# Kernel tuning notes

Measured on AMD Instinct MI355X. Metric: run time of the kernel, lower is better.

## Reference

```python
import jax, jax.numpy as jnp
import numpy as np

MAX_TOKENS = 8192
MAX_NUM_NODES = 8192
FEATURES = 256


def setup_inputs() -> dict:
    key = jax.random.key(0)
    k_emb, k_start, k_end = jax.random.split(key, 3)
    embedding = jax.random.normal(k_emb, (MAX_NUM_NODES, FEATURES), dtype=jnp.float32)
    node_span_starts = jax.random.randint(k_start, (MAX_NUM_NODES,), 0, 4096, dtype=jnp.int32)
    node_span_ends = jax.random.randint(k_end, (MAX_NUM_NODES,), 0, MAX_TOKENS, dtype=jnp.int32)
    return {
        "embedding": embedding,
        "node_span_starts": node_span_starts,
        "node_span_ends": node_span_ends,
        "num_nodes": 6000,
    }


def reference(embedding, node_span_starts, node_span_ends, num_nodes):
    # For each token t: out[t] = sum over valid nodes n with start_n <= t <= end_n of embedding[n].
    # Identical math to the original vmap+where+sum, expressed as a masked matmul
    # to avoid the O(N*T*F) dense intermediate.
    t = jnp.arange(MAX_TOKENS)[:, None]                      # [T, 1]
    node_valid = jnp.arange(MAX_NUM_NODES) < num_nodes       # [N]
    in_span = (node_span_starts[None, :] <= t) & (t <= node_span_ends[None, :])  # [T, N]
    mask = (in_span & node_valid[None, :]).astype(embedding.dtype)               # [T, N]
    return mask @ embedding                                  # [T, F]
```

## Files before the change

### kernel.cpp

```cpp
#include <hip/hip_runtime.h>

#define T_TOKENS 8192
#define MAX_NODES 8192
#define FEAT 256
#define NCHUNKS 1024
#define CHUNK 8
#define NSUPER 32
#define SUPER 32
#define LIST_CAP 4096
#define EV_STRIDE LIST_CAP

__global__ __launch_bounds__(FEAT) void classify_colsum_kernel(
    const float* __restrict__ emb,
    const int* __restrict__ starts,
    const int* __restrict__ ends,
    const int* __restrict__ num_nodes_p,
    float* __restrict__ colsum,
    float* __restrict__ supersum,
    int* __restrict__ evcnt,
    int* __restrict__ evbuf) {
    __shared__ int s_list[LIST_CAP];
    __shared__ int s_cnt;
    const int c = blockIdx.x;
    const int tid = threadIdx.x;
    const int f = tid;
    const int num_nodes = *num_nodes_p;
    const int row_lo = c * CHUNK;
    const int row_hi = row_lo + CHUNK;
    const int4* starts4 = (const int4*)starts;
    const int4* ends4 = (const int4*)ends;

    if (tid == 0) s_cnt = 0;
    __syncthreads();
#pragma unroll
    for (int r = 0; r < MAX_NODES / (4 * FEAT); ++r) {
        const int vec = r * FEAT + tid;
        const int4 s4 = starts4[vec];
        const int4 e4 = ends4[vec];
        const int sv[4] = {s4.x, s4.y, s4.z, s4.w};
        const int ev[4] = {e4.x, e4.y, e4.z, e4.w};
        const int nb = vec * 4;
#pragma unroll
        for (int k = 0; k < 4; ++k) {
            const int node = nb + k;
            const int s = sv[k];
            const int e = ev[k];
            if (node < num_nodes && s <= e && s < T_TOKENS && e >= 0) {
                const int sc = s < 0 ? 0 : s;
                if (sc >= row_lo && sc < row_hi) {
                    int p = atomicAdd(&s_cnt, 1);
                    if (p < LIST_CAP) s_list[p] = (node << 4) | ((sc - row_lo) << 1);
                }
                const int e1 = e + 1;
                if (e1 < T_TOKENS && e1 >= row_lo && e1 < row_hi) {
                    int p = atomicAdd(&s_cnt, 1);
                    if (p < LIST_CAP) s_list[p] = (node << 4) | ((e1 - row_lo) << 1) | 1;
                }
            }
        }
    }
    __syncthreads();
    const int cnt = min(s_cnt, LIST_CAP);

    int* evb = evbuf + (size_t)c * EV_STRIDE;
    for (int j = tid; j < cnt; j += FEAT) evb[j] = s_list[j];
    if (tid == 0) evcnt[c] = cnt;

    float acc = 0.f;
    int j = 0;
    for (; j + 8 <= cnt; j += 8) {
        const int e0 = s_list[j + 0], e1 = s_list[j + 1];
        const int e2 = s_list[j + 2], e3 = s_list[j + 3];
        const int e4_ = s_list[j + 4], e5 = s_list[j + 5];
        const int e6 = s_list[j + 6], e7 = s_list[j + 7];
        const float v0 = emb[(size_t)(e0 >> 4) * FEAT + f];
        const float v1 = emb[(size_t)(e1 >> 4) * FEAT + f];
        const float v2 = emb[(size_t)(e2 >> 4) * FEAT + f];
        const float v3 = emb[(size_t)(e3 >> 4) * FEAT + f];
        const float v4 = emb[(size_t)(e4_ >> 4) * FEAT + f];
        const float v5 = emb[(size_t)(e5 >> 4) * FEAT + f];
        const float v6 = emb[(size_t)(e6 >> 4) * FEAT + f];
        const float v7 = emb[(size_t)(e7 >> 4) * FEAT + f];
        acc += (e0 & 1) ? -v0 : v0;
        acc += (e1 & 1) ? -v1 : v1;
        acc += (e2 & 1) ? -v2 : v2;
        acc += (e3 & 1) ? -v3 : v3;
        acc += (e4_ & 1) ? -v4 : v4;
        acc += (e5 & 1) ? -v5 : v5;
        acc += (e6 & 1) ? -v6 : v6;
        acc += (e7 & 1) ? -v7 : v7;
    }
    for (; j < cnt; ++j) {
        const int e0 = s_list[j];
        const float v0 = emb[(size_t)(e0 >> 4) * FEAT + f];
        acc += (e0 & 1) ? -v0 : v0;
    }
    colsum[(size_t)c * FEAT + f] = acc;
    atomicAdd(&supersum[(size_t)(c >> 5) * FEAT + f], acc);
}

#define APPLY_EVENT(eV, vV)                          \
    {                                                \
        const float sv_ = ((eV) & 1) ? -(vV) : (vV); \
        const int lr_ = ((eV) >> 1) & 7;             \
        d0 += (lr_ == 0) ? sv_ : 0.f;                \
        d1 += (lr_ == 1) ? sv_ : 0.f;                \
        d2 += (lr_ == 2) ? sv_ : 0.f;                \
        d3 += (lr_ == 3) ? sv_ : 0.f;                \
        d4 += (lr_ == 4) ? sv_ : 0.f;                \
        d5 += (lr_ == 5) ? sv_ : 0.f;                \
        d6 += (lr_ == 6) ? sv_ : 0.f;                \
        d7 += (lr_ == 7) ? sv_ : 0.f;                \
    }

__global__ __launch_bounds__(FEAT) void scan_kernel(
    const float* __restrict__ emb,
    const float* __restrict__ colsum,
    const float* __restrict__ supersum,
    const int* __restrict__ evcnt,
    const int* __restrict__ evbuf,
    float* __restrict__ out) {
    const int c = blockIdx.x;
    const int f = threadIdx.x;
    const int sg = c >> 5;

    const int cnt = evcnt[c];
    const int* evb = evbuf + (size_t)c * EV_STRIDE;

    float r0 = 0.f, r1 = 0.f, r2 = 0.f, r3 = 0.f;
    float r4 = 0.f, r5 = 0.f, r6 = 0.f, r7 = 0.f;
    int i = 0;
    for (; i + 8 <= sg; i += 8) {
        r0 += supersum[(size_t)(i + 0) * FEAT + f];
        r1 += supersum[(size_t)(i + 1) * FEAT + f];
        r2 += supersum[(size_t)(i + 2) * FEAT + f];
        r3 += supersum[(size_t)(i + 3) * FEAT + f];
        r4 += supersum[(size_t)(i + 4) * FEAT + f];
        r5 += supersum[(size_t)(i + 5) * FEAT + f];
        r6 += supersum[(size_t)(i + 6) * FEAT + f];
        r7 += supersum[(size_t)(i + 7) * FEAT + f];
    }
    for (; i < sg; ++i) r0 += supersum[(size_t)i * FEAT + f];
    i = sg * SUPER;
    for (; i + 8 <= c; i += 8) {
        r0 += colsum[(size_t)(i + 0) * FEAT + f];
        r1 += colsum[(size_t)(i + 1) * FEAT + f];
        r2 += colsum[(size_t)(i + 2) * FEAT + f];
        r3 += colsum[(size_t)(i + 3) * FEAT + f];
        r4 += colsum[(size_t)(i + 4) * FEAT + f];
        r5 += colsum[(size_t)(i + 5) * FEAT + f];
        r6 += colsum[(size_t)(i + 6) * FEAT + f];
        r7 += colsum[(size_t)(i + 7) * FEAT + f];
    }
    for (; i < c; ++i) r0 += colsum[(size_t)i * FEAT + f];
    float run = ((r0 + r1) + (r2 + r3)) + ((r4 + r5) + (r6 + r7));

    float d0 = 0.f, d1 = 0.f, d2 = 0.f, d3 = 0.f;
    float d4 = 0.f, d5 = 0.f, d6 = 0.f, d7 = 0.f;
    int j = 0;
    for (; j + 4 <= cnt; j += 4) {
        const int e0 = evb[j + 0], e1 = evb[j + 1];
        const int e2 = evb[j + 2], e3 = evb[j + 3];
        const float v0 = emb[(size_t)(e0 >> 4) * FEAT + f];
        const float v1 = emb[(size_t)(e1 >> 4) * FEAT + f];
        const float v2 = emb[(size_t)(e2 >> 4) * FEAT + f];
        const float v3 = emb[(size_t)(e3 >> 4) * FEAT + f];
        APPLY_EVENT(e0, v0);
        APPLY_EVENT(e1, v1);
        APPLY_EVENT(e2, v2);
        APPLY_EVENT(e3, v3);
    }
    for (; j < cnt; ++j) {
        const int e0 = evb[j];
        const float v0 = emb[(size_t)(e0 >> 4) * FEAT + f];
        APPLY_EVENT(e0, v0);
    }

    float* o = out + (size_t)c * CHUNK * FEAT + f;
    run += d0; o[0 * FEAT] = run;
    run += d1; o[1 * FEAT] = run;
    run += d2; o[2 * FEAT] = run;
    run += d3; o[3 * FEAT] = run;
    run += d4; o[4 * FEAT] = run;
    run += d5; o[5 * FEAT] = run;
    run += d6; o[6 * FEAT] = run;
    run += d7; o[7 * FEAT] = run;
}

extern "C" void kernel_launch(void* const* d_in, const int* in_sizes, int n_in,
                              void* d_out, int out_size, void* d_ws, size_t ws_size,
                              hipStream_t stream) {
    const float* emb     = (const float*)d_in[0];
    const int* starts    = (const int*)d_in[1];
    const int* ends      = (const int*)d_in[2];
    const int* num_nodes = (const int*)d_in[3];
    float* out           = (float*)d_out;

    float* colsum   = (float*)d_ws;
    float* supersum = colsum + (size_t)NCHUNKS * FEAT;
    int* evcnt      = (int*)(supersum + (size_t)NSUPER * FEAT);
    int* evbuf      = evcnt + NCHUNKS;

    hipMemsetAsync(supersum, 0, (size_t)NSUPER * FEAT * sizeof(float), stream);

    classify_colsum_kernel<<<NCHUNKS, FEAT, 0, stream>>>(
        emb, starts, ends, num_nodes, colsum, supersum, evcnt, evbuf);
    scan_kernel<<<NCHUNKS, FEAT, 0, stream>>>(
        emb, colsum, supersum, evcnt, evbuf, out);
}
```

Before: 84.19 us.

## Fuse classify and scan into one cooperative kernel with grid syncs

Replaces the memset plus two-kernel pipeline with a single cooperative kernel. Each block keeps its event list in shared memory and its per-row deltas in registers, so it no longer writes events to global memory, re-reads them, or gathers embedding rows a second time. Supersums are computed after a grid sync instead of with atomics. The trade-off is two grid-wide barriers and a requirement that all 1024 blocks be co-resident; if the occupancy check or the cooperative launch fails, it falls back to the old path.

```diff
diff --git a/kernel.cpp b/kernel.cpp
--- a/kernel.cpp
+++ b/kernel.cpp
@@ -1,4 +1,7 @@
 #include <hip/hip_runtime.h>
+#include <hip/hip_cooperative_groups.h>
+
+namespace cg = cooperative_groups;
 
 #define T_TOKENS 8192
 #define MAX_NODES 8192
@@ -9,6 +12,167 @@
 #define SUPER 32
 #define LIST_CAP 4096
 #define EV_STRIDE LIST_CAP
+
+#define APPLY_EVENT(eV, vV)                          \
+    {                                                \
+        const float sv_ = ((eV) & 1) ? -(vV) : (vV); \
+        const int lr_ = ((eV) >> 1) & 7;             \
+        d0 += (lr_ == 0) ? sv_ : 0.f;                \
+        d1 += (lr_ == 1) ? sv_ : 0.f;                \
+        d2 += (lr_ == 2) ? sv_ : 0.f;                \
+        d3 += (lr_ == 3) ? sv_ : 0.f;                \
+        d4 += (lr_ == 4) ? sv_ : 0.f;                \
+        d5 += (lr_ == 5) ? sv_ : 0.f;                \
+        d6 += (lr_ == 6) ? sv_ : 0.f;                \
+        d7 += (lr_ == 7) ? sv_ : 0.f;                \
+    }
+
+__global__ __launch_bounds__(FEAT, 4) void fused_kernel(
+    const float* __restrict__ emb,
+    const int* __restrict__ starts,
+    const int* __restrict__ ends,
+    const int* __restrict__ num_nodes_p,
+    float* __restrict__ colsum,
+    float* __restrict__ supersum,
+    float* __restrict__ out) {
+    __shared__ int s_list[LIST_CAP];
+    __shared__ int s_cnt;
+    const int c = blockIdx.x;
+    const int tid = threadIdx.x;
+    const int f = tid;
+    const int num_nodes = *num_nodes_p;
+    const int row_lo = c * CHUNK;
+    const int row_hi = row_lo + CHUNK;
+    const int4* starts4 = (const int4*)starts;
+    const int4* ends4 = (const int4*)ends;
+
+    if (tid == 0) s_cnt = 0;
+    __syncthreads();
+#pragma unroll
+    for (int r = 0; r < MAX_NODES / (4 * FEAT); ++r) {
+        const int vec = r * FEAT + tid;
+        const int4 s4 = starts4[vec];
+        const int4 e4 = ends4[vec];
+        const int sv[4] = {s4.x, s4.y, s4.z, s4.w};
+        const int ev[4] = {e4.x, e4.y, e4.z, e4.w};
+        const int nb = vec * 4;
+#pragma unroll
+        for (int k = 0; k < 4; ++k) {
+            const int node = nb + k;
+            const int s = sv[k];
+            const int e = ev[k];
+            if (node < num_nodes && s <= e && s < T_TOKENS && e >= 0) {
+                const int sc = s < 0 ? 0 : s;
+                if (sc >= row_lo && sc < row_hi) {
+                    int p = atomicAdd(&s_cnt, 1);
+                    if (p < LIST_CAP) s_list[p] = (node << 4) | ((sc - row_lo) << 1);
+                }
+                const int e1 = e + 1;
+                if (e1 < T_TOKENS && e1 >= row_lo && e1 < row_hi) {
+                    int p = atomicAdd(&s_cnt, 1);
+                    if (p < LIST_CAP) s_list[p] = (node << 4) | ((e1 - row_lo) << 1) | 1;
+                }
+            }
+        }
+    }
+    __syncthreads();
+    const int cnt = min(s_cnt, LIST_CAP);
+
+    float d0 = 0.f, d1 = 0.f, d2 = 0.f, d3 = 0.f;
+    float d4 = 0.f, d5 = 0.f, d6 = 0.f, d7 = 0.f;
+    {
+        int j = 0;
+        for (; j + 8 <= cnt; j += 8) {
+            const int e0 = s_list[j + 0], e1 = s_list[j + 1];
+            const int e2 = s_list[j + 2], e3 = s_list[j + 3];
+            const int e4_ = s_list[j + 4], e5 = s_list[j + 5];
+            const int e6 = s_list[j + 6], e7 = s_list[j + 7];
+            const float v0 = emb[(size_t)(e0 >> 4) * FEAT + f];
+            const float v1 = emb[(size_t)(e1 >> 4) * FEAT + f];
+            const float v2 = emb[(size_t)(e2 >> 4) * FEAT + f];
+            const float v3 = emb[(size_t)(e3 >> 4) * FEAT + f];
+            const float v4 = emb[(size_t)(e4_ >> 4) * FEAT + f];
+            const float v5 = emb[(size_t)(e5 >> 4) * FEAT + f];
+            const float v6 = emb[(size_t)(e6 >> 4) * FEAT + f];
+            const float v7 = emb[(size_t)(e7 >> 4) * FEAT + f];
+            APPLY_EVENT(e0, v0);
+            APPLY_EVENT(e1, v1);
+            APPLY_EVENT(e2, v2);
+            APPLY_EVENT(e3, v3);
+            APPLY_EVENT(e4_, v4);
+            APPLY_EVENT(e5, v5);
+            APPLY_EVENT(e6, v6);
+            APPLY_EVENT(e7, v7);
+        }
+        for (; j < cnt; ++j) {
+            const int e0 = s_list[j];
+            const float v0 = emb[(size_t)(e0 >> 4) * FEAT + f];
+            APPLY_EVENT(e0, v0);
+        }
+    }
+    colsum[(size_t)c * FEAT + f] = ((d0 + d1) + (d2 + d3)) + ((d4 + d5) + (d6 + d7));
+
+    cg::this_grid().sync();
+
+    if (c < NSUPER) {
+        const float* cs = colsum + (size_t)c * SUPER * FEAT + f;
+        float t0 = 0.f, t1 = 0.f, t2 = 0.f, t3 = 0.f;
+        float t4 = 0.f, t5 = 0.f, t6 = 0.f, t7 = 0.f;
+#pragma unroll
+        for (int j = 0; j < SUPER; j += 8) {
+            t0 += cs[(size_t)(j + 0) * FEAT];
+            t1 += cs[(size_t)(j + 1) * FEAT];
+            t2 += cs[(size_t)(j + 2) * FEAT];
+            t3 += cs[(size_t)(j + 3) * FEAT];
+            t4 += cs[(size_t)(j + 4) * FEAT];
+            t5 += cs[(size_t)(j + 5) * FEAT];
+            t6 += cs[(size_t)(j + 6) * FEAT];
+            t7 += cs[(size_t)(j + 7) * FEAT];
+        }
+        supersum[(size_t)c * FEAT + f] = ((t0 + t1) + (t2 + t3)) + ((t4 + t5) + (t6 + t7));
+    }
+
+    cg::this_grid().sync();
+
+    const int sg = c >> 5;
+    float r0 = 0.f, r1 = 0.f, r2 = 0.f, r3 = 0.f;
+    float r4 = 0.f, r5 = 0.f, r6 = 0.f, r7 = 0.f;
+    int i = 0;
+    for (; i + 8 <= sg; i += 8) {
+        r0 += supersum[(size_t)(i + 0) * FEAT + f];
+        r1 += supersum[(size_t)(i + 1) * FEAT + f];
+        r2 += supersum[(size_t)(i + 2) * FEAT + f];
+        r3 += supersum[(size_t)(i + 3) * FEAT + f];
+        r4 += supersum[(size_t)(i + 4) * FEAT + f];
+        r5 += supersum[(size_t)(i + 5) * FEAT + f];
+        r6 += supersum[(size_t)(i + 6) * FEAT + f];
+        r7 += supersum[(size_t)(i + 7) * FEAT + f];
+    }
+    for (; i < sg; ++i) r0 += supersum[(size_t)i * FEAT + f];
+    i = sg * SUPER;
+    for (; i + 8 <= c; i += 8) {
+        r0 += colsum[(size_t)(i + 0) * FEAT + f];
+        r1 += colsum[(size_t)(i + 1) * FEAT + f];
+        r2 += colsum[(size_t)(i + 2) * FEAT + f];
+        r3 += colsum[(size_t)(i + 3) * FEAT + f];
+        r4 += colsum[(size_t)(i + 4) * FEAT + f];
+        r5 += colsum[(size_t)(i + 5) * FEAT + f];
+        r6 += colsum[(size_t)(i + 6) * FEAT + f];
+        r7 += colsum[(size_t)(i + 7) * FEAT + f];
+    }
+    for (; i < c; ++i) r0 += colsum[(size_t)i * FEAT + f];
+    float run = ((r0 + r1) + (r2 + r3)) + ((r4 + r5) + (r6 + r7));
+
+    float* o = out + (size_t)c * CHUNK * FEAT + f;
+    run += d0; o[0 * FEAT] = run;
+    run += d1; o[1 * FEAT] = run;
+    run += d2; o[2 * FEAT] = run;
+    run += d3; o[3 * FEAT] = run;
+    run += d4; o[4 * FEAT] = run;
+    run += d5; o[5 * FEAT] = run;
+    run += d6; o[6 * FEAT] = run;
+    run += d7; o[7 * FEAT] = run;
+}
 
 __global__ __launch_bounds__(FEAT) void classify_colsum_kernel(
     const float* __restrict__ emb,
@@ -99,20 +263,6 @@
     atomicAdd(&supersum[(size_t)(c >> 5) * FEAT + f], acc);
 }
 
-#define APPLY_EVENT(eV, vV)                          \
-    {                                                \
-        const float sv_ = ((eV) & 1) ? -(vV) : (vV); \
-        const int lr_ = ((eV) >> 1) & 7;             \
-        d0 += (lr_ == 0) ? sv_ : 0.f;                \
-        d1 += (lr_ == 1) ? sv_ : 0.f;                \
-        d2 += (lr_ == 2) ? sv_ : 0.f;                \
-        d3 += (lr_ == 3) ? sv_ : 0.f;                \
-        d4 += (lr_ == 4) ? sv_ : 0.f;                \
-        d5 += (lr_ == 5) ? sv_ : 0.f;                \
-        d6 += (lr_ == 6) ? sv_ : 0.f;                \
-        d7 += (lr_ == 7) ? sv_ : 0.f;                \
-    }
-
 __global__ __launch_bounds__(FEAT) void scan_kernel(
     const float* __restrict__ emb,
     const float* __restrict__ colsum,
@@ -190,6 +340,7 @@
 extern "C" void kernel_launch(void* const* d_in, const int* in_sizes, int n_in,
                               void* d_out, int out_size, void* d_ws, size_t ws_size,
                               hipStream_t stream) {
+    (void)in_sizes; (void)n_in; (void)out_size; (void)ws_size;
     const float* emb     = (const float*)d_in[0];
     const int* starts    = (const int*)d_in[1];
     const int* ends      = (const int*)d_in[2];
@@ -201,8 +352,23 @@
     int* evcnt      = (int*)(supersum + (size_t)NSUPER * FEAT);
     int* evbuf      = evcnt + NCHUNKS;
 
+    static int s_coop = -1;
+    if (s_coop < 0) {
+        int nb = 0;
+        hipError_t oe = hipOccupancyMaxActiveBlocksPerMultiprocessor(&nb, fused_kernel, FEAT, 0);
+        s_coop = (oe == hipSuccess && nb > 0 && nb * 256 >= NCHUNKS) ? 1 : 0;
+    }
+
+    if (s_coop == 1) {
+        void* args[] = {(void*)&emb, (void*)&starts, (void*)&ends, (void*)&num_nodes,
+                        (void*)&colsum, (void*)&supersum, (void*)&out};
+        hipError_t le = hipLaunchCooperativeKernel(fused_kernel, dim3(NCHUNKS), dim3(FEAT),
+                                                   args, 0, stream);
+        if (le == hipSuccess) return;
+        s_coop = 0;
+    }
+
     hipMemsetAsync(supersum, 0, (size_t)NSUPER * FEAT * sizeof(float), stream);
-
     classify_colsum_kernel<<<NCHUNKS, FEAT, 0, stream>>>(
         emb, starts, ends, num_nodes, colsum, supersum, evcnt, evbuf);
     scan_kernel<<<NCHUNKS, FEAT, 0, stream>>>(
```

New measurement: 315.2 us. +274.3%, slower.

## Fuse event gather into classify kernel and replace memset with flag-guarded zeroing

Applied to the files above, without the earlier changes.

The classify kernel now applies each chunk's start and end events directly into eight per-row accumulators and writes partial prefix rows to the output. The scan kernel only adds the cross-chunk running sum from colsum and supersum. This removes the second gather of embedding rows and the global event buffer round trip. The separate memset is replaced by in-kernel zeroing of supersum, guarded by a spin-wait on a release/acquire flag. The node scan stops at num_nodes, and the shared list capacity is halved. Risks: the flag is never reset between calls, so on later launches a block could add into supersum before the zeroing happens; the spin-wait also assumes the zeroing block gets scheduled; and the halved list capacity could overflow when many events fall in one chunk.

```diff
diff --git a/kernel.cpp b/kernel.cpp
--- a/kernel.cpp
+++ b/kernel.cpp
@@ -7,33 +7,78 @@
 #define CHUNK 8
 #define NSUPER 32
 #define SUPER 32
-#define LIST_CAP 4096
-#define EV_STRIDE LIST_CAP
-
-__global__ __launch_bounds__(FEAT) void classify_colsum_kernel(
+#define LIST_CAP 2048
+#define FLAG_STRIDE 16
+#define FLAG_MAGIC 0x1B7F00D5
+#define FLAG_PAD 64
+
+#define APPLY_EVENT(eV, vV)                          \
+    {                                                \
+        const float sv_ = ((eV) & 1) ? -(vV) : (vV); \
+        const int lr_ = ((eV) >> 1) & 7;             \
+        d0 += (lr_ == 0) ? sv_ : 0.f;                \
+        d1 += (lr_ == 1) ? sv_ : 0.f;                \
+        d2 += (lr_ == 2) ? sv_ : 0.f;                \
+        d3 += (lr_ == 3) ? sv_ : 0.f;                \
+        d4 += (lr_ == 4) ? sv_ : 0.f;                \
+        d5 += (lr_ == 5) ? sv_ : 0.f;                \
+        d6 += (lr_ == 6) ? sv_ : 0.f;                \
+        d7 += (lr_ == 7) ? sv_ : 0.f;                \
+    }
+
+__device__ __forceinline__ float sum_rows_plain(const float* p, int n, int f) {
+    float r0 = 0.f, r1 = 0.f, r2 = 0.f, r3 = 0.f;
+    float r4 = 0.f, r5 = 0.f, r6 = 0.f, r7 = 0.f;
+    int i = 0;
+    for (; i + 8 <= n; i += 8) {
+        r0 += p[(size_t)(i + 0) * FEAT + f];
+        r1 += p[(size_t)(i + 1) * FEAT + f];
+        r2 += p[(size_t)(i + 2) * FEAT + f];
+        r3 += p[(size_t)(i + 3) * FEAT + f];
+        r4 += p[(size_t)(i + 4) * FEAT + f];
+        r5 += p[(size_t)(i + 5) * FEAT + f];
+        r6 += p[(size_t)(i + 6) * FEAT + f];
+        r7 += p[(size_t)(i + 7) * FEAT + f];
+    }
+    for (; i < n; ++i) r0 += p[(size_t)i * FEAT + f];
+    return ((r0 + r1) + (r2 + r3)) + ((r4 + r5) + (r6 + r7));
+}
+
+__global__ __launch_bounds__(FEAT) void k1_classify(
     const float* __restrict__ emb,
     const int* __restrict__ starts,
     const int* __restrict__ ends,
     const int* __restrict__ num_nodes_p,
     float* __restrict__ colsum,
     float* __restrict__ supersum,
-    int* __restrict__ evcnt,
-    int* __restrict__ evbuf) {
+    int* __restrict__ sflag,
+    float* __restrict__ out,
+    int preset) {
     __shared__ int s_list[LIST_CAP];
     __shared__ int s_cnt;
     const int c = blockIdx.x;
     const int tid = threadIdx.x;
     const int f = tid;
+    const int sg = c >> 5;
+    const int lc = c & 31;
     const int num_nodes = *num_nodes_p;
     const int row_lo = c * CHUNK;
     const int row_hi = row_lo + CHUNK;
     const int4* starts4 = (const int4*)starts;
     const int4* ends4 = (const int4*)ends;
 
+    if (!preset && lc == 0) {
+        supersum[(size_t)sg * FEAT + f] = 0.f;
+        __syncthreads();
+        if (tid == 0)
+            __hip_atomic_store(&sflag[sg * FLAG_STRIDE], FLAG_MAGIC,
+                               __ATOMIC_RELEASE, __HIP_MEMORY_SCOPE_AGENT);
+    }
+
     if (tid == 0) s_cnt = 0;
     __syncthreads();
-#pragma unroll
-    for (int r = 0; r < MAX_NODES / (4 * FEAT); ++r) {
+    const int R = min(MAX_NODES / (4 * FEAT), (num_nodes + 1023) >> 10);
+    for (int r = 0; r < R; ++r) {
         const int vec = r * FEAT + tid;
         const int4 s4 = starts4[vec];
         const int4 e4 = ends4[vec];
@@ -62,121 +107,43 @@
     __syncthreads();
     const int cnt = min(s_cnt, LIST_CAP);
 
-    int* evb = evbuf + (size_t)c * EV_STRIDE;
-    for (int j = tid; j < cnt; j += FEAT) evb[j] = s_list[j];
-    if (tid == 0) evcnt[c] = cnt;
-
-    float acc = 0.f;
-    int j = 0;
-    for (; j + 8 <= cnt; j += 8) {
-        const int e0 = s_list[j + 0], e1 = s_list[j + 1];
-        const int e2 = s_list[j + 2], e3 = s_list[j + 3];
-        const int e4_ = s_list[j + 4], e5 = s_list[j + 5];
-        const int e6 = s_list[j + 6], e7 = s_list[j + 7];
-        const float v0 = emb[(size_t)(e0 >> 4) * FEAT + f];
-        const float v1 = emb[(size_t)(e1 >> 4) * FEAT + f];
-        const float v2 = emb[(size_t)(e2 >> 4) * FEAT + f];
-        const float v3 = emb[(size_t)(e3 >> 4) * FEAT + f];
-        const float v4 = emb[(size_t)(e4_ >> 4) * FEAT + f];
-        const float v5 = emb[(size_t)(e5 >> 4) * FEAT + f];
-        const float v6 = emb[(size_t)(e6 >> 4) * FEAT + f];
-        const float v7 = emb[(size_t)(e7 >> 4) * FEAT + f];
-        acc += (e0 & 1) ? -v0 : v0;
-        acc += (e1 & 1) ? -v1 : v1;
-        acc += (e2 & 1) ? -v2 : v2;
-        acc += (e3 & 1) ? -v3 : v3;
-        acc += (e4_ & 1) ? -v4 : v4;
-        acc += (e5 & 1) ? -v5 : v5;
-        acc += (e6 & 1) ? -v6 : v6;
-        acc += (e7 & 1) ? -v7 : v7;
-    }
-    for (; j < cnt; ++j) {
-        const int e0 = s_list[j];
-        const float v0 = emb[(size_t)(e0 >> 4) * FEAT + f];
-        acc += (e0 & 1) ? -v0 : v0;
-    }
-    colsum[(size_t)c * FEAT + f] = acc;
-    atomicAdd(&supersum[(size_t)(c >> 5) * FEAT + f], acc);
-}
-
-#define APPLY_EVENT(eV, vV)                          \
-    {                                                \
-        const float sv_ = ((eV) & 1) ? -(vV) : (vV); \
-        const int lr_ = ((eV) >> 1) & 7;             \
-        d0 += (lr_ == 0) ? sv_ : 0.f;                \
-        d1 += (lr_ == 1) ? sv_ : 0.f;                \
-        d2 += (lr_ == 2) ? sv_ : 0.f;                \
-        d3 += (lr_ == 3) ? sv_ : 0.f;                \
-        d4 += (lr_ == 4) ? sv_ : 0.f;                \
-        d5 += (lr_ == 5) ? sv_ : 0.f;                \
-        d6 += (lr_ == 6) ? sv_ : 0.f;                \
-        d7 += (lr_ == 7) ? sv_ : 0.f;                \
-    }
-
-__global__ __launch_bounds__(FEAT) void scan_kernel(
-    const float* __restrict__ emb,
-    const float* __restrict__ colsum,
-    const float* __restrict__ supersum,
-    const int* __restrict__ evcnt,
-    const int* __restrict__ evbuf,
-    float* __restrict__ out) {
-    const int c = blockIdx.x;
-    const int f = threadIdx.x;
-    const int sg = c >> 5;
-
-    const int cnt = evcnt[c];
-    const int* evb = evbuf + (size_t)c * EV_STRIDE;
-
-    float r0 = 0.f, r1 = 0.f, r2 = 0.f, r3 = 0.f;
-    float r4 = 0.f, r5 = 0.f, r6 = 0.f, r7 = 0.f;
-    int i = 0;
-    for (; i + 8 <= sg; i += 8) {
-        r0 += supersum[(size_t)(i + 0) * FEAT + f];
-        r1 += supersum[(size_t)(i + 1) * FEAT + f];
-        r2 += supersum[(size_t)(i + 2) * FEAT + f];
-        r3 += supersum[(size_t)(i + 3) * FEAT + f];
-        r4 += supersum[(size_t)(i + 4) * FEAT + f];
-        r5 += supersum[(size_t)(i + 5) * FEAT + f];
-        r6 += supersum[(size_t)(i + 6) * FEAT + f];
-        r7 += supersum[(size_t)(i + 7) * FEAT + f];
-    }
-    for (; i < sg; ++i) r0 += supersum[(size_t)i * FEAT + f];
-    i = sg * SUPER;
-    for (; i + 8 <= c; i += 8) {
-        r0 += colsum[(size_t)(i + 0) * FEAT + f];
-        r1 += colsum[(size_t)(i + 1) * FEAT + f];
-        r2 += colsum[(size_t)(i + 2) * FEAT + f];
-        r3 += colsum[(size_t)(i + 3) * FEAT + f];
-        r4 += colsum[(size_t)(i + 4) * FEAT + f];
-        r5 += colsum[(size_t)(i + 5) * FEAT + f];
-        r6 += colsum[(size_t)(i + 6) * FEAT + f];
-        r7 += colsum[(size_t)(i + 7) * FEAT + f];
-    }
-    for (; i < c; ++i) r0 += colsum[(size_t)i * FEAT + f];
-    float run = ((r0 + r1) + (r2 + r3)) + ((r4 + r5) + (r6 + r7));
-
     float d0 = 0.f, d1 = 0.f, d2 = 0.f, d3 = 0.f;
     float d4 = 0.f, d5 = 0.f, d6 = 0.f, d7 = 0.f;
-    int j = 0;
-    for (; j + 4 <= cnt; j += 4) {
-        const int e0 = evb[j + 0], e1 = evb[j + 1];
-        const int e2 = evb[j + 2], e3 = evb[j + 3];
-        const float v0 = emb[(size_t)(e0 >> 4) * FEAT + f];
-        const float v1 = emb[(size_t)(e1 >> 4) * FEAT + f];
-        const float v2 = emb[(size_t)(e2 >> 4) * FEAT + f];
-        const float v3 = emb[(size_t)(e3 >> 4) * FEAT + f];
-        APPLY_EVENT(e0, v0);
-        APPLY_EVENT(e1, v1);
-        APPLY_EVENT(e2, v2);
-        APPLY_EVENT(e3, v3);
-    }
-    for (; j < cnt; ++j) {
-        const int e0 = evb[j];
-        const float v0 = emb[(size_t)(e0 >> 4) * FEAT + f];
-        APPLY_EVENT(e0, v0);
-    }
+    {
+        int j = 0;
+        for (; j + 8 <= cnt; j += 8) {
+            const int e0 = s_list[j + 0], e1 = s_list[j + 1];
+            const int e2 = s_list[j + 2], e3 = s_list[j + 3];
+            const int e4_ = s_list[j + 4], e5 = s_list[j + 5];
+            const int e6 = s_list[j + 6], e7 = s_list[j + 7];
+            const float v0 = emb[(size_t)(e0 >> 4) * FEAT + f];
+            const float v1 = emb[(size_t)(e1 >> 4) * FEAT + f];
+            const float v2 = emb[(size_t)(e2 >> 4) * FEAT + f];
+            const float v3 = emb[(size_t)(e3 >> 4) * FEAT + f];
+            const float v4 = emb[(size_t)(e4_ >> 4) * FEAT + f];
+            const float v5 = emb[(size_t)(e5 >> 4) * FEAT + f];
+            const float v6 = emb[(size_t)(e6 >> 4) * FEAT + f];
+            const float v7 = emb[(size_t)(e7 >> 4) * FEAT + f];
+            APPLY_EVENT(e0, v0);
+            APPLY_EVENT(e1, v1);
+            APPLY_EVENT(e2, v2);
+            APPLY_EVENT(e3, v3);
+            APPLY_EVENT(e4_, v4);
+            APPLY_EVENT(e5, v5);
+            APPLY_EVENT(e6, v6);
+            APPLY_EVENT(e7, v7);
+        }
+        for (; j < cnt; ++j) {
+            const int e0 = s_list[j];
+            const float v0 = emb[(size_t)(e0 >> 4) * FEAT + f];
+            APPLY_EVENT(e0, v0);
+        }
+    }
+    const float csum = ((d0 + d1) + (d2 + d3)) + ((d4 + d5) + (d6 + d7));
+    colsum[(size_t)c * FEAT + f] = csum;
 
     float* o = out + (size_t)c * CHUNK * FEAT + f;
+    float run = 0.f;
     run += d0; o[0 * FEAT] = run;
     run += d1; o[1 * FEAT] = run;
     run += d2; o[2 * FEAT] = run;
@@ -185,26 +152,77 @@
     run += d5; o[5 * FEAT] = run;
     run += d6; o[6 * FEAT] = run;
     run += d7; o[7 * FEAT] = run;
+
+    if (!preset) {
+        while (__hip_atomic_load(&sflag[sg * FLAG_STRIDE],
+                                 __ATOMIC_RELAXED, __HIP_MEMORY_SCOPE_AGENT) != FLAG_MAGIC)
+            __builtin_amdgcn_s_sleep(2);
+        __builtin_amdgcn_fence(__ATOMIC_ACQUIRE, "agent");
+    }
+    atomicAdd(&supersum[(size_t)sg * FEAT + f], csum);
+}
+
+__global__ __launch_bounds__(FEAT) void k2_scan(
+    const float* __restrict__ colsum,
+    const float* __restrict__ supersum,
+    float* __restrict__ out) {
+    const int c = blockIdx.x;
+    const int f = threadIdx.x;
+    const int sg = c >> 5;
+    const int lc = c & 31;
+
+    const float run = sum_rows_plain(supersum, sg, f) +
+                      sum_rows_plain(colsum + (size_t)sg * SUPER * FEAT, lc, f);
+
+    float* o = out + (size_t)c * CHUNK * FEAT + f;
+    const float v0 = o[0 * FEAT];
+    const float v1 = o[1 * FEAT];
+    const float v2 = o[2 * FEAT];
+    const float v3 = o[3 * FEAT];
+    const float v4 = o[4 * FEAT];
+    const float v5 = o[5 * FEAT];
+    const float v6 = o[6 * FEAT];
+    const float v7 = o[7 * FEAT];
+    o[0 * FEAT] = run + v0;
+    o[1 * FEAT] = run + v1;
+    o[2 * FEAT] = run + v2;
+    o[3 * FEAT] = run + v3;
+    o[4 * FEAT] = run + v4;
+    o[5 * FEAT] = run + v5;
+    o[6 * FEAT] = run + v6;
+    o[7 * FEAT] = run + v7;
 }
 
 extern "C" void kernel_launch(void* const* d_in, const int* in_sizes, int n_in,
                               void* d_out, int out_size, void* d_ws, size_t ws_size,
                               hipStream_t stream) {
+    (void)in_sizes; (void)n_in; (void)out_size; (void)ws_size;
     const float* emb     = (const float*)d_in[0];
     const int* starts    = (const int*)d_in[1];
     const int* ends      = (const int*)d_in[2];
     const int* num_nodes = (const int*)d_in[3];
     float* out           = (float*)d_out;
 
-    float* colsum   = (float*)d_ws;
+    int* sflag      = (int*)d_ws;
+    float* colsum   = (float*)(sflag + NSUPER * FLAG_STRIDE + FLAG_PAD);
     float* supersum = colsum + (size_t)NCHUNKS * FEAT;
-    int* evcnt      = (int*)(supersum + (size_t)NSUPER * FEAT);
-    int* evbuf      = evcnt + NCHUNKS;
-
-    hipMemsetAsync(supersum, 0, (size_t)NSUPER * FEAT * sizeof(float), stream);
-
-    classify_colsum_kernel<<<NCHUNKS, FEAT, 0, stream>>>(
-        emb, starts, ends, num_nodes, colsum, supersum, evcnt, evbuf);
-    scan_kernel<<<NCHUNKS, FEAT, 0, stream>>>(
-        emb, colsum, supersum, evcnt, evbuf, out);
-}
+
+    static int s_ok = -1;
+    if (s_ok < 0) {
+        int nb = 0;
+        hipError_t oe = hipOccupancyMaxActiveBlocksPerMultiprocessor(&nb, k1_classify, FEAT, 0);
+        s_ok = (oe == hipSuccess && nb >= 4) ? 1 : 0;
+    }
+
+    if (s_ok == 1) {
+        k1_classify<<<NCHUNKS, FEAT, 0, stream>>>(
+            emb, starts, ends, num_nodes, colsum, supersum, sflag, out, 0);
+        k2_scan<<<NCHUNKS, FEAT, 0, stream>>>(colsum, supersum, out);
+        return;
+    }
+
+    (void)hipMemsetAsync(supersum, 0, (size_t)NSUPER * FEAT * sizeof(float), stream);
+    k1_classify<<<NCHUNKS, FEAT, 0, stream>>>(
+        emb, starts, ends, num_nodes, colsum, supersum, sflag, out, 1);
+    k2_scan<<<NCHUNKS, FEAT, 0, stream>>>(colsum, supersum, out);
+}
```

After: 109.7 us. +30.2%, slower.
